# Kernel optimization log

Hardware: AMD Instinct MI355X
Metric: run time of the kernel (lower is better)

Reference implementation:

```python
import jax, jax.numpy as jnp
import numpy as np
from math import pi

N = 262144
OUT_RES = 512
OUT_CHANNELS = 64
EPS = 3.33  # out_res in [177, 890)
SQ2PI = 2.50662827463


def make_sphere_pos(out_res, eps):
    # Fibonacci sphere lattice, matches the torch buffer construction.
    indices = jnp.arange(out_res, dtype=jnp.float32)
    golden_ratio = (1 + 5 ** 0.5) / 2
    phi = jnp.arccos(1 - 2 * (indices + eps) / (out_res - 1 + 2 * eps))
    theta = 2 * pi * indices / golden_ratio
    x = jnp.cos(theta) * jnp.sin(phi)
    y = jnp.sin(theta) * jnp.sin(phi)
    z = jnp.cos(phi)
    return jnp.stack([x, y, z], axis=0).astype(jnp.float32)  # [3, out_res]


def setup_inputs() -> dict:
    key = jax.random.key(0)
    k1, k2 = jax.random.split(key)
    vec = jax.random.normal(k1, (N, 3), dtype=jnp.float32)
    vec = vec / (jnp.linalg.norm(vec, axis=-1, keepdims=True) + 1e-8)  # unit directions
    weights = jax.random.uniform(k2, (1, OUT_RES, OUT_CHANNELS), dtype=jnp.float32)
    sphere_pos = make_sphere_pos(OUT_RES, EPS)
    sigma = jnp.full((1,), 0.1, dtype=jnp.float32)
    return {"vec": vec, "sphere_pos": sphere_pos, "weights": weights, "sigma": sigma}


def reference(vec, sphere_pos, weights, sigma):
    # cos_dist: [N, out_res]
    cos_dist = jnp.clip(vec @ sphere_pos, -1 + 1e-5, 1 - 1e-5)
    ang = jnp.arccos(cos_dist)
    prob = jnp.exp(-(ang / sigma) ** 2 / 2) / SQ2PI / sigma  # gaussian of geodesic dist
    prob = prob / (prob.sum(axis=1, keepdims=True) + 1e-8)
    # [N, out_res] @ [out_res, out_channels] -> [N, out_channels]
    return prob @ weights[0]
```

## Files before the change

kernel.cpp:

```cpp
#include <hip/hip_runtime.h>

typedef short bf16x8 __attribute__((ext_vector_type(8)));
typedef float f32x4  __attribute__((ext_vector_type(4)));

__device__ __forceinline__ unsigned short f2bf_rne(float x) {
  union { float f; unsigned u; } a; a.f = x;
  unsigned r = a.u + 0x7fffu + ((a.u >> 16) & 1u);
  return (unsigned short)(r >> 16);
}

__device__ __forceinline__ float fast_exp2(float x) {
#if __has_builtin(__builtin_amdgcn_exp2f)
  return __builtin_amdgcn_exp2f(x);
#else
  float r; asm("v_exp_f32 %0, %1" : "=v"(r) : "v"(x)); return r;
#endif
}

__device__ __forceinline__ unsigned cvt_pk_bf16(float a, float b) {
  unsigned r; asm("v_cvt_pk_bf16_f32 %0, %1, %2" : "=v"(r) : "v"(a), "v"(b)); return r;
}

__global__ __launch_bounds__(1024, 8) void sph_enc_kernel(
    const float* __restrict__ vec,
    const float* __restrict__ sph,
    const float* __restrict__ wts,
    const float* __restrict__ sigp,
    float* __restrict__ out)
{
  __shared__ __align__(16) unsigned char wlds[64 * 512 * 2];
  __shared__ __align__(16) float slds[3 * 512];

  const int tid  = threadIdx.x;
  const int lane = tid & 63;
  const int wave = tid >> 6;

  for (int i = tid; i < 1536; i += 1024) slds[i] = sph[i];

  {
    const int c    = tid & 63;
    const int kgrp = tid >> 6;
    const int swz  = (c & 7) << 4;
    #pragma unroll
    for (int pass = 0; pass < 4; ++pass) {
      const int k0 = pass * 128 + (kgrp << 3);
      unsigned pk[4];
      #pragma unroll
      for (int i = 0; i < 4; ++i) {
        const unsigned lo = f2bf_rne(wts[(k0 + 2 * i)     * 64 + c]);
        const unsigned hi = f2bf_rne(wts[(k0 + 2 * i + 1) * 64 + c]);
        pk[i] = lo | (hi << 16);
      }
      *reinterpret_cast<uint4*>(wlds + (((c << 10) + (k0 << 1)) ^ swz)) =
          make_uint4(pk[0], pk[1], pk[2], pk[3]);
    }
  }
  __syncthreads();

  const float sigma = sigp[0];
  const float C1 = -1.44269504f / (sigma * sigma);
  const float C2 = C1 * 0.16666667f;
  const float K2 = -__log2f(2.50662827463f * sigma);

  const int r16  = lane & 15;
  const int q    = lane >> 4;
  const int grow = (blockIdx.x << 8) + (wave << 4) + r16;

  const float nvx = -vec[grow * 3 + 0];
  const float nvy = -vec[grow * 3 + 1];
  const float nvz = -vec[grow * 3 + 2];

  f32x4 acc[4];
  #pragma unroll
  for (int nb = 0; nb < 4; ++nb) acc[nb] = (f32x4){0.f, 0.f, 0.f, 0.f};
  float rsa = 0.0f, rsb = 0.0f;

  const int swz_r = (lane & 7) << 4;

  #pragma unroll
  for (int kt = 0; kt < 16; ++kt) {
    const int j0 = kt * 32 + q * 8;
    union { bf16x8 v; unsigned u32[4]; } af;

    #pragma unroll
    for (int h = 0; h < 2; ++h) {
      const int jh = j0 + 4 * h;
      const f32x4 X = *reinterpret_cast<const f32x4*>(&slds[jh]);
      const f32x4 Y = *reinterpret_cast<const f32x4*>(&slds[512 + jh]);
      const f32x4 Z = *reinterpret_cast<const f32x4*>(&slds[1024 + jh]);
      float p[4];
      #pragma unroll
      for (int e = 0; e < 4; ++e) {
        const float u = fmaf(nvx, X[e], fmaf(nvy, Y[e], fmaf(nvz, Z[e], 1.0f)));
        p[e] = fast_exp2(fmaf(u, fmaf(u, C2, C1), K2));
      }
      rsa += p[0] + p[2];
      rsb += p[1] + p[3];
      af.u32[2 * h]     = cvt_pk_bf16(p[0], p[1]);
      af.u32[2 * h + 1] = cvt_pk_bf16(p[2], p[3]);
    }

    const int kbyte = j0 << 1;
    #pragma unroll
    for (int nb = 0; nb < 4; ++nb) {
      const bf16x8 bf = *reinterpret_cast<const bf16x8*>(
          wlds + (((((nb << 4) + r16) << 10) + kbyte) ^ swz_r));
      acc[nb] = __builtin_amdgcn_mfma_f32_16x16x32_bf16(af.v, bf, acc[nb], 0, 0, 0);
    }
  }

  float rsum = rsa + rsb;
  rsum += __shfl_xor(rsum, 16);
  rsum += __shfl_xor(rsum, 32);

  #pragma unroll
  for (int reg = 0; reg < 4; ++reg) {
    const int orow = (q << 2) + reg;
    const float rs   = __shfl(rsum, orow);
    const float rinv = 1.0f / (rs + 1e-8f);
    const int base = (((blockIdx.x << 8) + (wave << 4) + orow) << 6) + r16;
    out[base +  0] = acc[0][reg] * rinv;
    out[base + 16] = acc[1][reg] * rinv;
    out[base + 32] = acc[2][reg] * rinv;
    out[base + 48] = acc[3][reg] * rinv;
  }
}

extern "C" void kernel_launch(void* const* d_in, const int* in_sizes, int n_in,
                              void* d_out, int out_size, void* d_ws, size_t ws_size,
                              hipStream_t stream) {
  const float* vec = (const float*)d_in[0];
  const float* sph = (const float*)d_in[1];
  const float* wts = (const float*)d_in[2];
  const float* sig = (const float*)d_in[3];
  float* out = (float*)d_out;
  const int n      = in_sizes[0] / 3;
  const int blocks = n >> 8;
  hipLaunchKernelGGL(sph_enc_kernel, dim3(blocks), dim3(1024), 0, stream,
                     vec, sph, wts, sig, out);
}
```

Measured before the change: 51.84 us.

## Process two 16-row tiles per wave to amortize weight staging and LDS reads

Each wave now computes two independent 16-row M tiles that share the same sphere-position and weight B-fragment LDS loads, and the grid is halved to 512 rows per block. This halves the number of blocks that convert and stage the 64KB weight matrix into LDS, and it halves the B-operand LDS traffic per row. In exchange it doubles accumulator and probability registers per thread and lowers the launch-bounds occupancy hint, so fewer blocks are available to hide latency.

```diff
diff --git a/kernel.cpp b/kernel.cpp
--- a/kernel.cpp
+++ b/kernel.cpp
@@ -21,7 +21,7 @@
   unsigned r; asm("v_cvt_pk_bf16_f32 %0, %1, %2" : "=v"(r) : "v"(a), "v"(b)); return r;
 }
 
-__global__ __launch_bounds__(1024, 8) void sph_enc_kernel(
+__global__ __launch_bounds__(1024, 4) void sph_enc_kernel(
     const float* __restrict__ vec,
     const float* __restrict__ sph,
     const float* __restrict__ wts,
@@ -64,23 +64,30 @@
 
   const int r16  = lane & 15;
   const int q    = lane >> 4;
-  const int grow = (blockIdx.x << 8) + (wave << 4) + r16;
+  const int row0 = (blockIdx.x << 9) + (wave << 4) + r16;
+  const int row1 = row0 + 256;
 
-  const float nvx = -vec[grow * 3 + 0];
-  const float nvy = -vec[grow * 3 + 1];
-  const float nvz = -vec[grow * 3 + 2];
+  const float nvx0 = -vec[row0 * 3 + 0];
+  const float nvy0 = -vec[row0 * 3 + 1];
+  const float nvz0 = -vec[row0 * 3 + 2];
+  const float nvx1 = -vec[row1 * 3 + 0];
+  const float nvy1 = -vec[row1 * 3 + 1];
+  const float nvz1 = -vec[row1 * 3 + 2];
 
-  f32x4 acc[4];
+  f32x4 acc0[4], acc1[4];
   #pragma unroll
-  for (int nb = 0; nb < 4; ++nb) acc[nb] = (f32x4){0.f, 0.f, 0.f, 0.f};
-  float rsa = 0.0f, rsb = 0.0f;
+  for (int nb = 0; nb < 4; ++nb) {
+    acc0[nb] = (f32x4){0.f, 0.f, 0.f, 0.f};
+    acc1[nb] = (f32x4){0.f, 0.f, 0.f, 0.f};
+  }
+  float rsa0 = 0.f, rsb0 = 0.f, rsa1 = 0.f, rsb1 = 0.f;
 
   const int swz_r = (lane & 7) << 4;
 
   #pragma unroll
   for (int kt = 0; kt < 16; ++kt) {
     const int j0 = kt * 32 + q * 8;
-    union { bf16x8 v; unsigned u32[4]; } af;
+    union { bf16x8 v; unsigned u32[4]; } af0, af1;
 
     #pragma unroll
     for (int h = 0; h < 2; ++h) {
@@ -91,13 +98,22 @@
       float p[4];
       #pragma unroll
       for (int e = 0; e < 4; ++e) {
-        const float u = fmaf(nvx, X[e], fmaf(nvy, Y[e], fmaf(nvz, Z[e], 1.0f)));
+        const float u = fmaf(nvx0, X[e], fmaf(nvy0, Y[e], fmaf(nvz0, Z[e], 1.0f)));
         p[e] = fast_exp2(fmaf(u, fmaf(u, C2, C1), K2));
       }
-      rsa += p[0] + p[2];
-      rsb += p[1] + p[3];
-      af.u32[2 * h]     = cvt_pk_bf16(p[0], p[1]);
-      af.u32[2 * h + 1] = cvt_pk_bf16(p[2], p[3]);
+      rsa0 += p[0] + p[2];
+      rsb0 += p[1] + p[3];
+      af0.u32[2 * h]     = cvt_pk_bf16(p[0], p[1]);
+      af0.u32[2 * h + 1] = cvt_pk_bf16(p[2], p[3]);
+      #pragma unroll
+      for (int e = 0; e < 4; ++e) {
+        const float u = fmaf(nvx1, X[e], fmaf(nvy1, Y[e], fmaf(nvz1, Z[e], 1.0f)));
+        p[e] = fast_exp2(fmaf(u, fmaf(u, C2, C1), K2));
+      }
+      rsa1 += p[0] + p[2];
+      rsb1 += p[1] + p[3];
+      af1.u32[2 * h]     = cvt_pk_bf16(p[0], p[1]);
+      af1.u32[2 * h + 1] = cvt_pk_bf16(p[2], p[3]);
     }
 
     const int kbyte = j0 << 1;
@@ -105,24 +121,34 @@
     for (int nb = 0; nb < 4; ++nb) {
       const bf16x8 bf = *reinterpret_cast<const bf16x8*>(
           wlds + (((((nb << 4) + r16) << 10) + kbyte) ^ swz_r));
-      acc[nb] = __builtin_amdgcn_mfma_f32_16x16x32_bf16(af.v, bf, acc[nb], 0, 0, 0);
+      acc0[nb] = __builtin_amdgcn_mfma_f32_16x16x32_bf16(af0.v, bf, acc0[nb], 0, 0, 0);
+      acc1[nb] = __builtin_amdgcn_mfma_f32_16x16x32_bf16(af1.v, bf, acc1[nb], 0, 0, 0);
     }
   }
 
-  float rsum = rsa + rsb;
-  rsum += __shfl_xor(rsum, 16);
-  rsum += __shfl_xor(rsum, 32);
+  float rsum0 = rsa0 + rsb0;
+  float rsum1 = rsa1 + rsb1;
+  rsum0 += __shfl_xor(rsum0, 16);
+  rsum0 += __shfl_xor(rsum0, 32);
+  rsum1 += __shfl_xor(rsum1, 16);
+  rsum1 += __shfl_xor(rsum1, 32);
 
+  const int obase = (blockIdx.x << 9) + (wave << 4);
   #pragma unroll
   for (int reg = 0; reg < 4; ++reg) {
     const int orow = (q << 2) + reg;
-    const float rs   = __shfl(rsum, orow);
-    const float rinv = 1.0f / (rs + 1e-8f);
-    const int base = (((blockIdx.x << 8) + (wave << 4) + orow) << 6) + r16;
-    out[base +  0] = acc[0][reg] * rinv;
-    out[base + 16] = acc[1][reg] * rinv;
-    out[base + 32] = acc[2][reg] * rinv;
-    out[base + 48] = acc[3][reg] * rinv;
+    const float rinv0 = 1.0f / (__shfl(rsum0, orow) + 1e-8f);
+    const float rinv1 = 1.0f / (__shfl(rsum1, orow) + 1e-8f);
+    const int b0 = ((obase + orow) << 6) + r16;
+    const int b1 = ((obase + 256 + orow) << 6) + r16;
+    out[b0 +  0] = acc0[0][reg] * rinv0;
+    out[b0 + 16] = acc0[1][reg] * rinv0;
+    out[b0 + 32] = acc0[2][reg] * rinv0;
+    out[b0 + 48] = acc0[3][reg] * rinv0;
+    out[b1 +  0] = acc1[0][reg] * rinv1;
+    out[b1 + 16] = acc1[1][reg] * rinv1;
+    out[b1 + 32] = acc1[2][reg] * rinv1;
+    out[b1 + 48] = acc1[3][reg] * rinv1;
   }
 }
 
@@ -135,7 +161,7 @@
   const float* sig = (const float*)d_in[3];
   float* out = (float*)d_out;
   const int n      = in_sizes[0] / 3;
-  const int blocks = n >> 8;
+  const int blocks = n >> 9;
   hipLaunchKernelGGL(sph_enc_kernel, dim3(blocks), dim3(1024), 0, stream,
                      vec, sph, wts, sig, out);
 }
```

Result: faster. 48.96 us (-5.6%).
